# Kernel tuning notes

Hardware: AMD Instinct MI355X
Metric: run time of the kernel (lower is better)

Reference implementation:

```python
import jax, jax.numpy as jnp
import numpy as np

B, S, D = 2, 2048, 1024
N_HEADS = 16
HEAD_DIM = D // N_HEADS  # 64, even for RoPE
THETA = 10000.0


def rope_tables(seq, head_dim, dtype=jnp.float32):
    half = head_dim // 2
    freqs = 1.0 / (THETA ** (jnp.arange(half, dtype=jnp.float32) / half))
    angles = jnp.arange(seq, dtype=jnp.float32)[:, None] * freqs[None, :]  # [S, half]
    return jnp.cos(angles).astype(dtype), jnp.sin(angles).astype(dtype)


def apply_rope_interleaved(x, cos, sin):
    # x: [b, h, s, d]; even/odd interleaving
    x_even = x[..., 0::2]
    x_odd = x[..., 1::2]
    r_even = x_even * cos - x_odd * sin
    r_odd = x_even * sin + x_odd * cos
    # interleave back: stack on last axis then reshape
    out = jnp.stack([r_even, r_odd], axis=-1).reshape(x.shape)
    return out


def setup_inputs() -> dict:
    key = jax.random.key(0)
    ks = jax.random.split(key, 6)
    scale = 1.0 / np.sqrt(D)
    return {
        "x": jax.random.normal(ks[0], (B, S, D), dtype=jnp.float32),
        "Wq": jax.random.normal(ks[1], (D, D), dtype=jnp.float32) * scale,
        "Wk": jax.random.normal(ks[2], (D, D), dtype=jnp.float32) * scale,
        "Wv": jax.random.normal(ks[3], (D, D), dtype=jnp.float32) * scale,
        "Wo": jax.random.normal(ks[4], (D, D), dtype=jnp.float32) * scale,
        "bo": jnp.zeros((D,), dtype=jnp.float32),
    }


def reference(x, Wq, Wk, Wv, Wo, bo):
    b, s, _ = x.shape
    # QKV projections (no bias), split heads -> [b, h, s, hd]
    def proj(W):
        return jnp.einsum('bsd,de->bse', x, W).reshape(b, s, N_HEADS, HEAD_DIM).transpose(0, 2, 1, 3)
    q, k, v = proj(Wq), proj(Wk), proj(Wv)

    cos, sin = rope_tables(s, HEAD_DIM, x.dtype)  # [s, hd//2]
    q = apply_rope_interleaved(q, cos, sin)
    k = apply_rope_interleaved(k, cos, sin)

    scale = 1.0 / jnp.sqrt(jnp.asarray(HEAD_DIM, dtype=x.dtype))
    scores = jnp.einsum('bhqd,bhkd->bhqk', q, k) * scale  # [b, h, s, s]
    causal = jnp.tril(jnp.ones((s, s), dtype=bool))
    scores = jnp.where(causal[None, None], scores, jnp.asarray(-jnp.inf, dtype=scores.dtype))
    attn = jax.nn.softmax(scores, axis=-1)
    ctx = jnp.einsum('bhqk,bhkd->bhqd', attn, v)  # [b, h, s, hd]
    ctx = ctx.transpose(0, 2, 1, 3).reshape(b, s, N_HEADS * HEAD_DIM)
    return jnp.einsum('bsd,de->bse', ctx, Wo) + bo
```

## Files before the change

### kernel.cpp

```cpp
#include <hip/hip_runtime.h>
#include <hip/hip_bf16.h>
#include <math.h>

constexpr int Bb   = 2;
constexpr int S    = 2048;
constexpr int D    = 1024;
constexpr int H    = 16;
constexpr int Dh   = 64;
constexpr int HALF = 32;
constexpr int M    = Bb * S;
constexpr int K    = 1024;
constexpr int N    = 1024;

typedef __attribute__((ext_vector_type(8))) short short8;
typedef __attribute__((ext_vector_type(4))) float f32x4;

__device__ __forceinline__ unsigned short f2bf(float f) {
    unsigned int u = __float_as_uint(f);
    unsigned int r = (u + 0x7fffu + ((u >> 16) & 1u)) >> 16;
    return (unsigned short)r;
}

__device__ __forceinline__ void gl_lds16(const unsigned short* g, unsigned short* lds_base) {
    __builtin_amdgcn_global_load_lds(
        (const __attribute__((address_space(1))) unsigned int*)g,
        (__attribute__((address_space(3))) unsigned int*)lds_base, 16, 0, 0);
}

__global__ __launch_bounds__(256) void prep_kernel(
    const float* __restrict__ x,
    const float* W0, const float* W1, const float* W2, const float* W3,
    unsigned short* __restrict__ xb,
    unsigned short* T0, unsigned short* T1, unsigned short* T2, unsigned short* T3,
    float* __restrict__ cosT, float* __restrict__ sinT)
{
    __shared__ float tile[64][65];
    const int bid = blockIdx.x;
    const int tid = threadIdx.x;

    if (bid < 256) {
        int idx = bid * 256 + tid;
        int s = idx >> 5;
        int i = idx & 31;
        double freq = exp(-(double)i * (log(10000.0) / 32.0));
        double ang  = (double)s * freq;
        cosT[idx] = (float)cos(ang);
        sinT[idx] = (float)sin(ang);
    } else if (bid < 256 + 4096) {
        size_t i = (size_t)(bid - 256) * 256 + tid;
        float4 v = *(const float4*)(x + i * 4);
        ushort4 pk;
        pk.x = f2bf(v.x); pk.y = f2bf(v.y); pk.z = f2bf(v.z); pk.w = f2bf(v.w);
        *(ushort4*)(xb + i * 4) = pk;
    } else {
        int wb = bid - 4352;
        int z  = wb >> 8;
        int rem = wb & 255;
        const float* W = (z == 0) ? W0 : (z == 1) ? W1 : (z == 2) ? W2 : W3;
        unsigned short* T = (z == 0) ? T0 : (z == 1) ? T1 : (z == 2) ? T2 : T3;
        const int bk = (rem >> 4) * 64;
        const int bn = (rem & 15) * 64;
        const int lr = tid >> 4;
        const int lc = (tid & 15) * 4;

        #pragma unroll
        for (int i = 0; i < 4; ++i) {
            int r = lr + i * 16;
            float4 v = *(const float4*)(W + (size_t)(bk + r) * N + bn + lc);
            tile[r][lc + 0] = v.x; tile[r][lc + 1] = v.y;
            tile[r][lc + 2] = v.z; tile[r][lc + 3] = v.w;
        }
        __syncthreads();
        #pragma unroll
        for (int i = 0; i < 4; ++i) {
            int nr = lr + i * 16;
            ushort4 pk;
            pk.x = f2bf(tile[lc + 0][nr]);
            pk.y = f2bf(tile[lc + 1][nr]);
            pk.z = f2bf(tile[lc + 2][nr]);
            pk.w = f2bf(tile[lc + 3][nr]);
            *(ushort4*)(T + (size_t)(bn + nr) * K + bk + lc) = pk;
        }
    }
}

__global__ __launch_bounds__(512, 2) void gemm_qkv_kernel(
    const unsigned short* __restrict__ A,
    const unsigned short* __restrict__ BT,
    unsigned short* outQ, unsigned short* outK, unsigned short* outV,
    const float* __restrict__ cosT, const float* __restrict__ sinT)
{
    constexpr int NT   = 32;
    constexpr int BUFS = 256 * 32;
    __shared__ __align__(16) unsigned short As[4 * BUFS];
    __shared__ __align__(16) unsigned short Bs[4 * BUFS];

    const int tid  = threadIdx.x;
    const int wid  = tid >> 6;
    const int lane = tid & 63;
    const int col  = lane & 15;
    const int quad = lane >> 4;
    const int wr   = wid >> 2;
    const int wc   = wid & 3;

    const int mbase = blockIdx.y * 256;
    const int nbase = blockIdx.x * 256;

    const int srow = lane >> 2;
    const int sch  = lane & 3;
    const unsigned short *pA0, *pA1, *pB0, *pB1;
    unsigned short *dA0, *dA1, *dB0, *dB1;
    {
        int r0 = wid * 16 + srow;
        int r1 = 128 + wid * 16 + srow;
        pA0 = A  + (size_t)(mbase + r0) * K + ((sch + (r0 >> 1)) & 3) * 8;
        pA1 = A  + (size_t)(mbase + r1) * K + ((sch + (r1 >> 1)) & 3) * 8;
        pB0 = BT + (size_t)(nbase + r0) * K + ((sch + (r0 >> 1)) & 3) * 8;
        pB1 = BT + (size_t)(nbase + r1) * K + ((sch + (r1 >> 1)) & 3) * 8;
        dA0 = &As[(wid * 16) * 32];
        dA1 = &As[(128 + wid * 16) * 32];
        dB0 = &Bs[(wid * 16) * 32];
        dB1 = &Bs[(128 + wid * 16) * 32];
    }

    int aoff[8], boff[4];
    #pragma unroll
    for (int f = 0; f < 8; ++f) {
        int r = wr * 128 + f * 16 + col;
        aoff[f] = r * 32 + ((quad - (r >> 1)) & 3) * 8;
    }
    #pragma unroll
    for (int n = 0; n < 4; ++n) {
        int r = wc * 64 + n * 16 + col;
        boff[n] = r * 32 + ((quad - (r >> 1)) & 3) * 8;
    }

    f32x4 acc[8][4];
    #pragma unroll
    for (int f = 0; f < 8; ++f)
        #pragma unroll
        for (int n = 0; n < 4; ++n) acc[f][n] = (f32x4)0.f;

    auto stageA = [&](int slot) {
        gl_lds16(pA0, dA0 + slot * BUFS); pA0 += 32;
        gl_lds16(pA1, dA1 + slot * BUFS); pA1 += 32;
    };
    auto stageB = [&](int slot) {
        gl_lds16(pB0, dB0 + slot * BUFS); pB0 += 32;
        gl_lds16(pB1, dB1 + slot * BUFS); pB1 += 32;
    };

    stageA(0); stageB(0);
    stageA(1); stageB(1);
    stageA(2); stageB(2);
    asm volatile("s_waitcnt vmcnt(8)" ::: "memory");
    __builtin_amdgcn_s_barrier();
    __builtin_amdgcn_sched_barrier(0);

    #pragma unroll 1
    for (int t = 0; t < NT; ++t) {
        const unsigned short* Ab = &As[(t & 3) * BUFS];
        const unsigned short* Bc = &Bs[(t & 3) * BUFS];
        const int nslot = (t + 3) & 3;
        short8 af[4], bf[4];

        #pragma unroll
        for (int i = 0; i < 4; ++i) af[i] = *(const short8*)&Ab[aoff[i]];
        #pragma unroll
        for (int n = 0; n < 4; ++n) bf[n] = *(const short8*)&Bc[boff[n]];
        if (t < NT - 3) stageA(nslot);
        __builtin_amdgcn_sched_barrier(0);
        __builtin_amdgcn_s_barrier();
        asm volatile("s_waitcnt lgkmcnt(0)" ::: "memory");
        __builtin_amdgcn_s_setprio(1);
        #pragma unroll
        for (int i = 0; i < 4; ++i)
            #pragma unroll
            for (int n = 0; n < 4; ++n)
                acc[i][n] = __builtin_amdgcn_mfma_f32_16x16x32_bf16(af[i], bf[n], acc[i][n], 0, 0, 0);
        __builtin_amdgcn_s_setprio(0);
        __builtin_amdgcn_sched_barrier(0);
        __builtin_amdgcn_s_barrier();
        __builtin_amdgcn_sched_barrier(0);

        #pragma unroll
        for (int i = 0; i < 4; ++i) af[i] = *(const short8*)&Ab[aoff[4 + i]];
        if (t < NT - 3) stageB(nslot);
        __builtin_amdgcn_sched_barrier(0);
        __builtin_amdgcn_s_barrier();
        asm volatile("s_waitcnt lgkmcnt(0)" ::: "memory");
        __builtin_amdgcn_s_setprio(1);
        #pragma unroll
        for (int i = 0; i < 4; ++i)
            #pragma unroll
            for (int n = 0; n < 4; ++n)
                acc[4 + i][n] = __builtin_amdgcn_mfma_f32_16x16x32_bf16(af[i], bf[n], acc[4 + i][n], 0, 0, 0);
        __builtin_amdgcn_s_setprio(0);
        if (t < NT - 3)       { asm volatile("s_waitcnt vmcnt(8)" ::: "memory"); }
        else if (t == NT - 3) { asm volatile("s_waitcnt vmcnt(4)" ::: "memory"); }
        else if (t == NT - 2) { asm volatile("s_waitcnt vmcnt(0)" ::: "memory"); }
        __builtin_amdgcn_s_barrier();
        __builtin_amdgcn_sched_barrier(0);
    }

    const int z = nbase >> 10;
    if (z < 2) {
        unsigned short* o = z ? outK : outQ;
        #pragma unroll
        for (int n = 0; n < 4; ++n) {
            int nl = (nbase & 1023) + wc * 64 + n * 16 + col;
            int h = nl >> 6, dh0 = nl & 63, p = dh0 >> 1;
            bool even = !(dh0 & 1);
            #pragma unroll
            for (int f = 0; f < 8; ++f)
                #pragma unroll
                for (int reg = 0; reg < 4; ++reg) {
                    int m_g = mbase + wr * 128 + f * 16 + quad * 4 + reg;
                    int b = m_g >> 11, s = m_g & 2047;
                    float v = acc[f][n][reg];
                    float part = __shfl_xor(v, 1, 64);
                    float c = cosT[s * HALF + p], sn = sinT[s * HALF + p];
                    float r = even ? (v * c - part * sn) : (v * c + part * sn);
                    o[((size_t)(b * H + h) * S + s) * Dh + dh0] = f2bf(r);
                }
        }
    } else {
        #pragma unroll
        for (int n = 0; n < 4; ++n) {
            int nl = (nbase & 1023) + wc * 64 + n * 16 + col;
            int h = nl >> 6, dh0 = nl & 63;
            #pragma unroll
            for (int f = 0; f < 8; ++f) {
                int m0 = mbase + wr * 128 + f * 16 + quad * 4;
                int b = m0 >> 11, s = m0 & 2047;
                ushort4 pk;
                pk.x = f2bf(acc[f][n][0]);
                pk.y = f2bf(acc[f][n][1]);
                pk.z = f2bf(acc[f][n][2]);
                pk.w = f2bf(acc[f][n][3]);
                *(ushort4*)&outV[((size_t)(b * H + h) * Dh + dh0) * S + s] = pk;
            }
        }
    }
}

__global__ __launch_bounds__(256) void gemm_out_kernel(
    const unsigned short* __restrict__ A,
    const unsigned short* __restrict__ BT,
    float* __restrict__ outO, const float* __restrict__ bias)
{
    constexpr int BK   = 64;
    constexpr int ABUF = 64 * BK;
    constexpr int BBUF = 64 * BK;
    __shared__ __align__(16) unsigned short As[2 * ABUF];
    __shared__ __align__(16) unsigned short Bs[2 * BBUF];

    const int tid  = threadIdx.x;
    const int wave = tid >> 6;
    const int lane = tid & 63;
    const int col  = lane & 15;
    const int quad = lane >> 4;
    const int wy   = wave >> 1;
    const int wx   = wave & 1;

    const int mbase = blockIdx.y * 64;
    const int nbase = blockIdx.x * 64;

    const int srow8 = lane >> 3;
    const int sch8  = lane & 7;

    const unsigned short *pA[2], *pB[2];
    unsigned short *dA[2], *dB[2];
    #pragma unroll
    for (int w = 0; w < 2; ++w) {
        int base = wave * 16 + w * 8;
        int tr = base + srow8;
        pA[w] = A  + (size_t)(mbase + tr) * K + ((sch8 + (tr >> 1)) & 7) * 8;
        pB[w] = BT + (size_t)(nbase + tr) * K + ((sch8 + (tr >> 1)) & 7) * 8;
        dA[w] = &As[base * BK];
        dB[w] = &Bs[base * BK];
    }

    int aoff[2][2], boff[2][2];
    #pragma unroll
    for (int ks = 0; ks < 2; ++ks) {
        #pragma unroll
        for (int mi = 0; mi < 2; ++mi) {
            int r = wy * 32 + mi * 16 + col;
            aoff[ks][mi] = r * BK + (((ks * 4 + quad) - (r >> 1)) & 7) * 8;
        }
        #pragma unroll
        for (int ni = 0; ni < 2; ++ni) {
            int r = wx * 32 + ni * 16 + col;
            boff[ks][ni] = r * BK + (((ks * 4 + quad) - (r >> 1)) & 7) * 8;
        }
    }

    f32x4 acc[2][2];
    #pragma unroll
    for (int mi = 0; mi < 2; ++mi)
        #pragma unroll
        for (int ni = 0; ni < 2; ++ni) acc[mi][ni] = (f32x4)0.f;

    auto stage = [&](int buf) {
        #pragma unroll
        for (int w = 0; w < 2; ++w) { gl_lds16(pA[w], dA[w] + buf * ABUF); pA[w] += BK; }
        #pragma unroll
        for (int w = 0; w < 2; ++w) { gl_lds16(pB[w], dB[w] + buf * BBUF); pB[w] += BK; }
    };
    auto compute = [&](int buf) {
        const unsigned short* Ac = &As[buf * ABUF];
        const unsigned short* Bc = &Bs[buf * BBUF];
        #pragma unroll
        for (int ks = 0; ks < 2; ++ks) {
            short8 af[2], bfr[2];
            #pragma unroll
            for (int mi = 0; mi < 2; ++mi) af[mi] = *(const short8*)&Ac[aoff[ks][mi]];
            #pragma unroll
            for (int ni = 0; ni < 2; ++ni) bfr[ni] = *(const short8*)&Bc[boff[ks][ni]];
            #pragma unroll
            for (int mi = 0; mi < 2; ++mi)
                #pragma unroll
                for (int ni = 0; ni < 2; ++ni)
                    acc[mi][ni] = __builtin_amdgcn_mfma_f32_16x16x32_bf16(af[mi], bfr[ni], acc[mi][ni], 0, 0, 0);
        }
    };

    stage(0);
    #pragma unroll 1
    for (int kk = 0; kk < 16; kk += 2) {
        __syncthreads();
        if (kk + 1 < 16) stage(1);
        compute(0);
        __syncthreads();
        if (kk + 2 < 16) stage(0);
        compute(1);
    }

    #pragma unroll
    for (int ni = 0; ni < 2; ++ni) {
        int n_g = nbase + wx * 32 + ni * 16 + col;
        float bv = bias[n_g];
        #pragma unroll
        for (int mi = 0; mi < 2; ++mi)
            #pragma unroll
            for (int reg = 0; reg < 4; ++reg) {
                int m_g = mbase + wy * 32 + mi * 16 + quad * 4 + reg;
                outO[(size_t)m_g * N + n_g] = acc[mi][ni][reg] + bv;
            }
    }
}

__global__ __launch_bounds__(256) void attn_mfma_kernel(
    const unsigned short* __restrict__ q, const unsigned short* __restrict__ k,
    const unsigned short* __restrict__ vt, unsigned short* __restrict__ ctx)
{
    constexpr int TSZ = 64 * 64;
    __shared__ __align__(16) unsigned short Ks[2 * TSZ];
    __shared__ __align__(16) unsigned short Vs[2 * TSZ];
    __shared__ __align__(16) unsigned short Ps[4][16 * 64];

    const int tid  = threadIdx.x;
    const int wave = tid >> 6;
    const int lane = tid & 63;
    const int col  = lane & 15;
    const int quad = lane >> 4;
    const int l8   = lane >> 3, cp = lane & 7;

    const int bh = blockIdx.y;
    const unsigned short* qb = q  + (size_t)bh * S * Dh;
    const unsigned short* kb = k  + (size_t)bh * S * Dh;
    const unsigned short* vb = vt + (size_t)bh * Dh * S;
    const int b = bh >> 4, h = bh & 15;

    unsigned short* dk0 = &Ks[(wave * 16 + 0) * 64];
    unsigned short* dk1 = &Ks[(wave * 16 + 8) * 64];
    unsigned short* dv0 = &Vs[(wave * 16 + 0) * 64];
    unsigned short* dv1 = &Vs[(wave * 16 + 8) * 64];

    int foff[2][4];
    #pragma unroll
    for (int ks = 0; ks < 2; ++ks)
        #pragma unroll
        for (int nt = 0; nt < 4; ++nt) {
            int r = nt * 16 + col;
            foff[ks][nt] = r * 64 + (((ks * 4 + quad) - r) & 7) * 8;
        }
    int poffW[4][4];
    #pragma unroll
    for (int nt = 0; nt < 4; ++nt)
        #pragma unroll
        for (int reg = 0; reg < 4; ++reg) {
            int row = quad * 4 + reg;
            poffW[nt][reg] = row * 64 + (((nt * 2 + (col >> 3)) ^ (row & 7)) << 3) + (col & 7);
        }
    int poffR[2];
    #pragma unroll
    for (int ks = 0; ks < 2; ++ks)
        poffR[ks] = col * 64 + (((ks * 4 + quad) ^ (col & 7)) << 3);

    for (int phase = 0; phase < 2; ++phase) {
        const int qt  = phase ? (31 - (int)blockIdx.x) : (int)blockIdx.x;
        const int wr0 = qt * 64 + wave * 16;

        const unsigned short *pk0, *pk1, *pv0, *pv1;
        {
            int r0 = wave * 16 + l8, r1 = r0 + 8;
            pk0 = kb + (size_t)r0 * Dh + ((cp + r0) & 7) * 8;
            pk1 = kb + (size_t)r1 * Dh + ((cp + r1) & 7) * 8;
            pv0 = vb + (size_t)r0 * S + ((cp + r0) & 7) * 8;
            pv1 = vb + (size_t)r1 * S + ((cp + r1) & 7) * 8;
        }

        auto stageKV = [&](int buf) {
            gl_lds16(pk0, dk0 + buf * TSZ); gl_lds16(pk1, dk1 + buf * TSZ);
            gl_lds16(pv0, dv0 + buf * TSZ); gl_lds16(pv1, dv1 + buf * TSZ);
            pk0 += 64 * Dh; pk1 += 64 * Dh; pv0 += 64; pv1 += 64;
        };

        __syncthreads();
        stageKV(0);

        short8 qfrag[2];
        #pragma unroll
        for (int ks = 0; ks < 2; ++ks)
            qfrag[ks] = *(const short8*)(qb + (size_t)(wr0 + col) * Dh + ks * 32 + quad * 8);

        f32x4 O[4];
        float lacc[4];
        #pragma unroll
        for (int nt = 0; nt < 4; ++nt) O[nt] = (f32x4)0.f;
        #pragma unroll
        for (int r = 0; r < 4; ++r) lacc[r] = 0.f;

        auto subtile = [&](const unsigned short* Kc, const unsigned short* Vc, int t) {
            f32x4 sacc[4];
            #pragma unroll
            for (int nt = 0; nt < 4; ++nt) sacc[nt] = (f32x4)0.f;
            #pragma unroll
            for (int ks = 0; ks < 2; ++ks)
                #pragma unroll
                for (int nt = 0; nt < 4; ++nt) {
                    short8 kf = *(const short8*)&Kc[foff[ks][nt]];
                    sacc[nt] = __builtin_amdgcn_mfma_f32_16x16x32_bf16(qfrag[ks], kf, sacc[nt], 0, 0, 0);
                }
            float pb[4][4];
            #pragma unroll
            for (int nt = 0; nt < 4; ++nt) {
                int key_l = nt * 16 + col;
                #pragma unroll
                for (int reg = 0; reg < 4; ++reg) {
                    float e = __builtin_amdgcn_exp2f(
                        fmaf(sacc[nt][reg], 0.18033688011112042f, -11.541560327111707f));
                    if (t == qt && key_l > wave * 16 + quad * 4 + reg) e = 0.f;
                    pb[nt][reg] = e;
                }
            }
            #pragma unroll
            for (int reg = 0; reg < 4; ++reg)
                lacc[reg] += (pb[0][reg] + pb[1][reg]) + (pb[2][reg] + pb[3][reg]);
            #pragma unroll
            for (int nt = 0; nt < 4; ++nt)
                #pragma unroll
                for (int reg = 0; reg < 4; ++reg)
                    Ps[wave][poffW[nt][reg]] = f2bf(pb[nt][reg]);
            #pragma unroll
            for (int ks = 0; ks < 2; ++ks) {
                short8 pf = *(const short8*)&Ps[wave][poffR[ks]];
                #pragma unroll
                for (int nt = 0; nt < 4; ++nt) {
                    short8 vf = *(const short8*)&Vc[foff[ks][nt]];
                    O[nt] = __builtin_amdgcn_mfma_f32_16x16x32_bf16(pf, vf, O[nt], 0, 0, 0);
                }
            }
        };

        for (int i = 0; i <= qt; ++i) {
            __syncthreads();
            if (i < qt) stageKV((i + 1) & 1);
            subtile(&Ks[(i & 1) * TSZ], &Vs[(i & 1) * TSZ], i);
        }

        #pragma unroll
        for (int reg = 0; reg < 4; ++reg) {
            float s = lacc[reg];
            #pragma unroll
            for (int off = 1; off <= 8; off <<= 1)
                s += __shfl_xor(s, off, 64);
            lacc[reg] = s;
        }

        #pragma unroll
        for (int reg = 0; reg < 4; ++reg) {
            float inv = 1.0f / lacc[reg];
            int rg = wr0 + quad * 4 + reg;
            unsigned short* dst = ctx + ((size_t)b * S + rg) * 1024 + h * 64 + col;
            #pragma unroll
            for (int nt = 0; nt < 4; ++nt)
                dst[nt * 16] = f2bf(O[nt][reg] * inv);
        }
    }
}

extern "C" void kernel_launch(void* const* d_in, const int* in_sizes, int n_in,
                              void* d_out, int out_size, void* d_ws, size_t ws_size,
                              hipStream_t stream) {
    const float* x  = (const float*)d_in[0];
    const float* Wq = (const float*)d_in[1];
    const float* Wk = (const float*)d_in[2];
    const float* Wv = (const float*)d_in[3];
    const float* Wo = (const float*)d_in[4];
    const float* bo = (const float*)d_in[5];
    float* out = (float*)d_out;

    const size_t MK  = (size_t)M * K;
    const size_t NK  = (size_t)N * K;
    const size_t QKV = (size_t)Bb * H * S * Dh;

    unsigned short* xb   = (unsigned short*)d_ws;
    unsigned short* WqT  = xb  + MK;
    unsigned short* WkT  = WqT + NK;
    unsigned short* WvT  = WkT + NK;
    unsigned short* WoT  = WvT + NK;
    unsigned short* qbuf = WoT + NK;
    unsigned short* kbuf = qbuf + QKV;
    unsigned short* vtb  = kbuf + QKV;
    unsigned short* ctxb = vtb  + QKV;
    float* cosT = (float*)(ctxb + QKV);
    float* sinT = cosT + (size_t)S * HALF;

    prep_kernel<<<5376, 256, 0, stream>>>(x, Wq, Wk, Wv, Wo,
                                          xb, WqT, WkT, WvT, WoT, cosT, sinT);

    gemm_qkv_kernel<<<dim3(12, 16), 512, 0, stream>>>(
        xb, WqT, qbuf, kbuf, vtb, cosT, sinT);

    attn_mfma_kernel<<<dim3(16, Bb * H), 256, 0, stream>>>(qbuf, kbuf, vtb, ctxb);

    gemm_out_kernel<<<dim3(16, 64), 256, 0, stream>>>(ctxb, WoT, out, bo);
}
```

Before: 189.3 us.

## Split attention key tiles across two blocks and add combine kernel

Each query-tile pair is now processed by two blocks, one taking even key tiles and one taking odd key tiles, which doubles the attention grid. Each block writes unnormalized fp32 partial outputs and row sums to workspace. A new combine kernel adds the two partials, normalizes them and writes the bf16 context. The aim is more parallel work per CU and shorter per-block causal loops, paid for with extra global traffic for the fp32 partials, one more kernel launch and a larger workspace.

Result: no change. 188.8 us (-0.3%).

```diff
diff --git a/kernel.cpp b/kernel.cpp
--- a/kernel.cpp
+++ b/kernel.cpp
@@ -353,7 +353,8 @@
 
 __global__ __launch_bounds__(256) void attn_mfma_kernel(
     const unsigned short* __restrict__ q, const unsigned short* __restrict__ k,
-    const unsigned short* __restrict__ vt, unsigned short* __restrict__ ctx)
+    const unsigned short* __restrict__ vt,
+    float* __restrict__ Opart, float* __restrict__ lpart)
 {
     constexpr int TSZ = 64 * 64;
     __shared__ __align__(16) unsigned short Ks[2 * TSZ];
@@ -367,11 +368,13 @@
     const int quad = lane >> 4;
     const int l8   = lane >> 3, cp = lane & 7;
 
+    const int pairh = blockIdx.x;
+    const int pair  = pairh >> 1;
+    const int hpar  = pairh & 1;
     const int bh = blockIdx.y;
     const unsigned short* qb = q  + (size_t)bh * S * Dh;
     const unsigned short* kb = k  + (size_t)bh * S * Dh;
     const unsigned short* vb = vt + (size_t)bh * Dh * S;
-    const int b = bh >> 4, h = bh & 15;
 
     unsigned short* dk0 = &Ks[(wave * 16 + 0) * 64];
     unsigned short* dk1 = &Ks[(wave * 16 + 8) * 64];
@@ -400,26 +403,26 @@
         poffR[ks] = col * 64 + (((ks * 4 + quad) ^ (col & 7)) << 3);
 
     for (int phase = 0; phase < 2; ++phase) {
-        const int qt  = phase ? (31 - (int)blockIdx.x) : (int)blockIdx.x;
+        const int qt  = phase ? (31 - pair) : pair;
         const int wr0 = qt * 64 + wave * 16;
 
         const unsigned short *pk0, *pk1, *pv0, *pv1;
         {
             int r0 = wave * 16 + l8, r1 = r0 + 8;
-            pk0 = kb + (size_t)r0 * Dh + ((cp + r0) & 7) * 8;
-            pk1 = kb + (size_t)r1 * Dh + ((cp + r1) & 7) * 8;
-            pv0 = vb + (size_t)r0 * S + ((cp + r0) & 7) * 8;
-            pv1 = vb + (size_t)r1 * S + ((cp + r1) & 7) * 8;
+            pk0 = kb + (size_t)(hpar * 64 + r0) * Dh + ((cp + r0) & 7) * 8;
+            pk1 = kb + (size_t)(hpar * 64 + r1) * Dh + ((cp + r1) & 7) * 8;
+            pv0 = vb + (size_t)r0 * S + hpar * 64 + ((cp + r0) & 7) * 8;
+            pv1 = vb + (size_t)r1 * S + hpar * 64 + ((cp + r1) & 7) * 8;
         }
 
         auto stageKV = [&](int buf) {
             gl_lds16(pk0, dk0 + buf * TSZ); gl_lds16(pk1, dk1 + buf * TSZ);
             gl_lds16(pv0, dv0 + buf * TSZ); gl_lds16(pv1, dv1 + buf * TSZ);
-            pk0 += 64 * Dh; pk1 += 64 * Dh; pv0 += 64; pv1 += 64;
+            pk0 += 128 * Dh; pk1 += 128 * Dh; pv0 += 128; pv1 += 128;
         };
 
         __syncthreads();
-        stageKV(0);
+        if (hpar <= qt) stageKV(0);
 
         short8 qfrag[2];
         #pragma unroll
@@ -475,10 +478,11 @@
             }
         };
 
-        for (int i = 0; i <= qt; ++i) {
+        int j = 0;
+        for (int i = hpar; i <= qt; i += 2, ++j) {
             __syncthreads();
-            if (i < qt) stageKV((i + 1) & 1);
-            subtile(&Ks[(i & 1) * TSZ], &Vs[(i & 1) * TSZ], i);
+            if (i + 2 <= qt) stageKV((j + 1) & 1);
+            subtile(&Ks[(j & 1) * TSZ], &Vs[(j & 1) * TSZ], i);
         }
 
         #pragma unroll
@@ -490,16 +494,43 @@
             lacc[reg] = s;
         }
 
+        const size_t pb_base = (size_t)(hpar * 32 + bh) * S;
         #pragma unroll
         for (int reg = 0; reg < 4; ++reg) {
-            float inv = 1.0f / lacc[reg];
             int rg = wr0 + quad * 4 + reg;
-            unsigned short* dst = ctx + ((size_t)b * S + rg) * 1024 + h * 64 + col;
+            float* op = Opart + (pb_base + rg) * 64 + col;
             #pragma unroll
             for (int nt = 0; nt < 4; ++nt)
-                dst[nt * 16] = f2bf(O[nt][reg] * inv);
-        }
-    }
+                op[nt * 16] = O[nt][reg];
+            if (col == 0)
+                lpart[pb_base + rg] = lacc[reg];
+        }
+    }
+}
+
+__global__ __launch_bounds__(256) void combine_kernel(
+    const float* __restrict__ Opart, const float* __restrict__ lpart,
+    unsigned short* __restrict__ ctx)
+{
+    int gid = blockIdx.x * 256 + threadIdx.x;
+    int bh  = gid >> 15;
+    int rem = gid & 32767;
+    int qr  = rem >> 4;
+    int dg  = (rem & 15) << 2;
+
+    size_t i0 = ((size_t)bh * S + qr) * 64 + dg;
+    size_t i1 = ((size_t)(32 + bh) * S + qr) * 64 + dg;
+    float4 a = *(const float4*)(Opart + i0);
+    float4 c = *(const float4*)(Opart + i1);
+    float inv = 1.0f / (lpart[(size_t)bh * S + qr] + lpart[(size_t)(32 + bh) * S + qr]);
+
+    int b = bh >> 4, hh = bh & 15;
+    ushort4 pk;
+    pk.x = f2bf((a.x + c.x) * inv);
+    pk.y = f2bf((a.y + c.y) * inv);
+    pk.z = f2bf((a.z + c.z) * inv);
+    pk.w = f2bf((a.w + c.w) * inv);
+    *(ushort4*)(ctx + ((size_t)b * S + qr) * 1024 + hh * 64 + dg) = pk;
 }
 
 extern "C" void kernel_launch(void* const* d_in, const int* in_sizes, int n_in,
@@ -526,8 +557,10 @@
     unsigned short* kbuf = qbuf + QKV;
     unsigned short* vtb  = kbuf + QKV;
     unsigned short* ctxb = vtb  + QKV;
-    float* cosT = (float*)(ctxb + QKV);
-    float* sinT = cosT + (size_t)S * HALF;
+    float* cosT  = (float*)(ctxb + QKV);
+    float* sinT  = cosT + (size_t)S * HALF;
+    float* Opart = sinT + (size_t)S * HALF;
+    float* lpart = Opart + (size_t)2 * 32 * S * 64;
 
     prep_kernel<<<5376, 256, 0, stream>>>(x, Wq, Wk, Wv, Wo,
                                           xb, WqT, WkT, WvT, WoT, cosT, sinT);
@@ -535,7 +568,9 @@
     gemm_qkv_kernel<<<dim3(12, 16), 512, 0, stream>>>(
         xb, WqT, qbuf, kbuf, vtb, cosT, sinT);
 
-    attn_mfma_kernel<<<dim3(16, Bb * H), 256, 0, stream>>>(qbuf, kbuf, vtb, ctxb);
+    attn_mfma_kernel<<<dim3(32, Bb * H), 256, 0, stream>>>(qbuf, kbuf, vtb, Opart, lpart);
+
+    combine_kernel<<<4096, 256, 0, stream>>>(Opart, lpart, ctxb);
 
     gemm_out_kernel<<<dim3(16, 64), 256, 0, stream>>>(ctxb, WoT, out, bo);
 }
```
